# Kernel tuning notes

Hardware: AMD Instinct MI355X
Metric: run time of the kernel (lower is better)

The kernel has to match this reference:

```python
import jax, jax.numpy as jnp
import numpy as np

N = 65536        # total points across batch
NS = 16          # nsample (kNN neighbors)
D = 64           # d_model
FF = 64          # dim_feedforward width
CIN = 16         # input feature channels
EPS = 1e-5       # BatchNorm eps


def _bn_relu(x, g, b):
    # BatchNorm1d in training mode: per-channel stats over (N, L); x: (N, C, L)
    m = x.mean(axis=(0, 2), keepdims=True)
    v = x.var(axis=(0, 2), keepdims=True)
    return jax.nn.relu((x - m) * jax.lax.rsqrt(v + EPS) * g[None, :, None] + b[None, :, None])


def _dknn_layer(xyz, feats, knn_idx, knn_empty,
                wq, bq, wk, bk, w1, g1, b1, w2, g2, b2, wo, go, bo):
    # nhead = 1 -> single head uses the full d_model split
    Q = feats @ wq + bq                        # (N, D)
    K = feats @ wk + bk                        # (N, D)
    Kx = jnp.concatenate([K, xyz], axis=1)     # use_xyz=True -> (N, D+3)
    Qx = jnp.concatenate([Q, xyz], axis=1)     # (N, D+3)
    Kg = jnp.transpose(Kx[knn_idx], (0, 2, 1))  # irregular gather -> (N, D+3, NS)
    Qe = Qx[:, :, None]                        # (N, D+3, 1)
    x = jnp.concatenate([Kg - Qe, jnp.broadcast_to(Qe, Kg.shape)], axis=1)  # (N, 2*(D+3), NS)
    x = jnp.where(knn_empty[:, None, None], 0.0, x)   # empty-ball masking
    x = _bn_relu(jnp.einsum('ncs,cf->nfs', x, w1), g1, b1)  # Conv1d k=1 == channel matmul
    x = _bn_relu(jnp.einsum('ncs,cf->nfs', x, w2), g2, b2)
    x = jnp.max(x, axis=2, keepdims=True)      # max-pool over neighbors -> (N, FF, 1)
    x = _bn_relu(jnp.einsum('ncs,cf->nfs', x, wo), go, bo)  # out_conv
    return x[:, :, 0]                          # (N, D)


def setup_inputs() -> dict:
    key = jax.random.key(0)
    ks = jax.random.split(key, 16)
    inp = {
        'src_xyz': jax.random.normal(ks[0], (N, 3), jnp.float32) * 20.0,
        'src_feats': jax.random.normal(ks[1], (N, CIN), jnp.float32),
        'knn_idx': jax.random.randint(ks[2], (N, NS), 0, N, jnp.int32),
        'knn_empty': jax.random.randint(ks[3], (N,), 0, 20, jnp.int32) == 0,
    }
    k = 4
    cin = CIN
    for i in range(2):
        s = 1.0 / np.sqrt(cin)
        inp[f'l{i}_wq'] = jax.random.normal(ks[k], (cin, D), jnp.float32) * s; k += 1
        inp[f'l{i}_bq'] = jnp.zeros((D,), jnp.float32)
        inp[f'l{i}_wk'] = jax.random.normal(ks[k], (cin, D), jnp.float32) * s; k += 1
        inp[f'l{i}_bk'] = jnp.zeros((D,), jnp.float32)
        c = 2 * (D + 3)
        inp[f'l{i}_w1'] = jax.random.normal(ks[k], (c, FF), jnp.float32) * np.sqrt(2.0 / c); k += 1
        inp[f'l{i}_g1'] = jnp.ones((FF,), jnp.float32)
        inp[f'l{i}_b1'] = jnp.zeros((FF,), jnp.float32)
        inp[f'l{i}_w2'] = jax.random.normal(ks[k], (FF, FF), jnp.float32) * np.sqrt(2.0 / FF); k += 1
        inp[f'l{i}_g2'] = jnp.ones((FF,), jnp.float32)
        inp[f'l{i}_b2'] = jnp.zeros((FF,), jnp.float32)
        inp[f'l{i}_wo'] = jax.random.normal(ks[k], (FF, D), jnp.float32) * np.sqrt(2.0 / FF); k += 1
        inp[f'l{i}_go'] = jnp.ones((D,), jnp.float32)
        inp[f'l{i}_bo'] = jnp.zeros((D,), jnp.float32)
        cin = D
    return inp


def reference(src_xyz, src_feats, knn_idx, knn_empty,
              l0_wq, l0_bq, l0_wk, l0_bk, l0_w1, l0_g1, l0_b1, l0_w2, l0_g2, l0_b2, l0_wo, l0_go, l0_bo,
              l1_wq, l1_bq, l1_wk, l1_bk, l1_w1, l1_g1, l1_b1, l1_w2, l1_g2, l1_b2, l1_wo, l1_go, l1_bo):
    f = _dknn_layer(src_xyz, src_feats, knn_idx, knn_empty,
                    l0_wq, l0_bq, l0_wk, l0_bk, l0_w1, l0_g1, l0_b1, l0_w2, l0_g2, l0_b2, l0_wo, l0_go, l0_bo)
    f = _dknn_layer(src_xyz, f, knn_idx, knn_empty,
                    l1_wq, l1_bq, l1_wk, l1_bk, l1_w1, l1_g1, l1_b1, l1_w2, l1_g2, l1_b2, l1_wo, l1_go, l1_bo)
    return f
```

## Files before the change

kernel.cpp:

```cpp
#include <hip/hip_runtime.h>
#include <cstdint>

#define NPTS 65536
#define NS 16
#define EPSV 1e-5f

typedef __attribute__((ext_vector_type(8))) short bf16x8;
typedef __attribute__((ext_vector_type(4))) float f32x4;
typedef __attribute__((ext_vector_type(4))) unsigned int u32x4;
union FragU { u32x4 u; bf16x8 h; };

#define SUM1 0
#define SSQ1 64
#define SUM2 128
#define SSQ2 192
#define SUM3 256
#define SSQ3 320
#define WKA_OFF 832
#define WQBA_OFF (832+4096)
#define BKA_OFF  (832+8192)
#define BQBA_OFF (832+8192+64)
#define STATS_FLOATS (832+8192+128)

__device__ __forceinline__ void split2(float e0, float e1, unsigned int& hi, unsigned int& lo) {
    unsigned int u0 = __float_as_uint(e0), u1 = __float_as_uint(e1);
    unsigned int h0 = u0 & 0xFFFF0000u, h1 = u1 & 0xFFFF0000u;
    hi = (h0 >> 16) | h1;
    float l0f = e0 - __uint_as_float(h0);
    float l1f = e1 - __uint_as_float(h1);
    lo = (__float_as_uint(l0f) >> 16) | (__float_as_uint(l1f) & 0xFFFF0000u);
}

__global__ void k_mask(const uint32_t* emp32, uint8_t* mask) {
    int bad = 0;
    for (int w = threadIdx.x; w < 1024; w += 256) bad |= (emp32[w] > 1u) ? 1 : 0;
    __shared__ int sbad[4];
    unsigned long long b = __ballot(bad != 0);
    if ((threadIdx.x & 63) == 0) sbad[threadIdx.x >> 6] = (b != 0ull) ? 1 : 0;
    __syncthreads();
    int flag = sbad[0] | sbad[1] | sbad[2] | sbad[3];
    int i = blockIdx.x * 256 + threadIdx.x;
    uint8_t mv;
    if (flag) mv = (((const uint8_t*)emp32)[i] != 0);
    else      mv = (emp32[i] != 0u);
    mask[i] = mv;
}

__global__ void k0(const float* wq, const float* bq, const float* wk, const float* bk,
                   const float* w1, float* stats, int cin) {
    int f = threadIdx.x;
    int c = blockIdx.x;
    float a = 0.f, q = 0.f;
    for (int d = 0; d < 64; d++) {
        float A  = w1[d*64 + f];
        float Bm = w1[(67+d)*64 + f] - A;
        a = fmaf(wk[c*64 + d], A,  a);
        q = fmaf(wq[c*64 + d], Bm, q);
    }
    stats[WKA_OFF  + c*64 + f] = a;
    stats[WQBA_OFF + c*64 + f] = q;
    if (c == 0) {
        float ba = 0.f, bqv = 0.f;
        for (int d = 0; d < 64; d++) {
            float A  = w1[d*64 + f];
            float Bm = w1[(67+d)*64 + f] - A;
            ba  = fmaf(bk[d], A,  ba);
            bqv = fmaf(bq[d], Bm, bqv);
        }
        stats[BKA_OFF  + f] = ba;
        stats[BQBA_OFF + f] = bqv;
    }
}

__global__ void k1(const float* feats, const float* xyz, const float* w1,
                   const float* stats, float* KA, float* QBA, int cin) {
    int t = blockIdx.x * 256 + threadIdx.x;
    int f = t & 63, n = t >> 6;
    const float* Wka  = stats + WKA_OFF;
    const float* Wqba = stats + WQBA_OFF;
    float ka = stats[BKA_OFF + f], qb = stats[BQBA_OFF + f];
    for (int c = 0; c < cin; c++) {
        float fv = feats[n*cin + c];
        ka = fmaf(fv, Wka[c*64 + f],  ka);
        qb = fmaf(fv, Wqba[c*64 + f], qb);
    }
    #pragma unroll
    for (int x = 0; x < 3; x++) {
        float xv = xyz[n*3 + x];
        float a  = w1[(64+x)*64 + f];
        ka = fmaf(xv, a, ka);
        qb = fmaf(xv, w1[(131+x)*64 + f] - a, qb);
    }
    KA[n*64 + f]  = ka;
    QBA[n*64 + f] = qb;
}

__global__ void k2(const float* KA, const float* QBA, const int* knn,
                   const uint8_t* mask, float* stats) {
    int lane = threadIdx.x & 63;
    int wv   = threadIdx.x >> 6;
    float s0 = 0.f, s1 = 0.f;
    for (int n = blockIdx.x * 4 + wv; n < NPTS; n += gridDim.x * 4) {
        float msk = mask[n] ? 0.0f : 1.0f;
        int myidx = knn[n*16 + (lane & 15)];
        float q = QBA[n*64 + lane];
        #pragma unroll
        for (int s = 0; s < 16; s++) {
            int j = __shfl(myidx, s, 64);
            float y = msk * (KA[j*64 + lane] + q);
            s0 += y;
            s1 = fmaf(y, y, s1);
        }
    }
    __shared__ float red[8][64];
    red[wv][lane] = s0;
    red[4+wv][lane] = s1;
    __syncthreads();
    if (wv == 0) {
        atomicAdd(&stats[SUM1 + lane], red[0][lane]+red[1][lane]+red[2][lane]+red[3][lane]);
        atomicAdd(&stats[SSQ1 + lane], red[4][lane]+red[5][lane]+red[6][lane]+red[7][lane]);
    }
}

__global__ void __launch_bounds__(256) k4(const float* KA, const float* QBA, const int* knn,
                   const uint8_t* mask, const float* w2, const float* g1, const float* b1,
                   float* stats, float* y2max, float* y2min) {
    const int l    = threadIdx.x & 63;
    const int wv   = threadIdx.x >> 6;
    const int sidx = l & 15;
    const int g    = l >> 4;
    const int col  = sidx;

    float sc1v[16], sh1v[16];
    const float inv = 1.0f / ((float)NPTS * (float)NS);
    #pragma unroll
    for (int t = 0; t < 2; t++)
    #pragma unroll
    for (int i = 0; i < 8; i++) {
        int c = t*32 + g*8 + i;
        float m = stats[SUM1 + c] * inv;
        float v = fmaxf(stats[SSQ1 + c] * inv - m*m, 0.0f);
        float s = g1[c] * rsqrtf(v + EPSV);
        sc1v[t*8+i] = s;
        sh1v[t*8+i] = fmaf(-m, s, b1[c]);
    }

    unsigned int whu[2][4][4], wlu[2][4][4];
    #pragma unroll
    for (int t = 0; t < 2; t++)
    #pragma unroll
    for (int ft = 0; ft < 4; ft++)
    #pragma unroll
    for (int r = 0; r < 4; r++) {
        int k0i = t*32 + g*8 + 2*r;
        float e0 = w2[k0i*64 + ft*16 + col];
        float e1 = w2[(k0i+1)*64 + ft*16 + col];
        split2(e0, e1, whu[t][ft][r], wlu[t][ft][r]);
    }

    float s0t[4] = {0.f,0.f,0.f,0.f};
    float s1t[4] = {0.f,0.f,0.f,0.f};

    for (int n = blockIdx.x * 4 + wv; n < NPTS; n += gridDim.x * 4) {
        bool masked = mask[n] != 0;
        int j = knn[n*16 + sidx];

        f32x4 kaA = *(const f32x4*)(KA + j*64 + g*8);
        f32x4 kaB = *(const f32x4*)(KA + j*64 + g*8 + 4);
        f32x4 kaC = *(const f32x4*)(KA + j*64 + 32 + g*8);
        f32x4 kaD = *(const f32x4*)(KA + j*64 + 32 + g*8 + 4);
        f32x4 qA  = *(const f32x4*)(QBA + n*64 + g*8);
        f32x4 qB  = *(const f32x4*)(QBA + n*64 + g*8 + 4);
        f32x4 qC  = *(const f32x4*)(QBA + n*64 + 32 + g*8);
        f32x4 qD  = *(const f32x4*)(QBA + n*64 + 32 + g*8 + 4);

        float x[16];
        #pragma unroll
        for (int i = 0; i < 4; i++) {
            float y0 = masked ? 0.f : (kaA[i] + qA[i]);
            float y1 = masked ? 0.f : (kaB[i] + qB[i]);
            float y2 = masked ? 0.f : (kaC[i] + qC[i]);
            float y3 = masked ? 0.f : (kaD[i] + qD[i]);
            x[i]    = fmaxf(fmaf(sc1v[i],    y0, sh1v[i]),    0.0f);
            x[4+i]  = fmaxf(fmaf(sc1v[4+i],  y1, sh1v[4+i]),  0.0f);
            x[8+i]  = fmaxf(fmaf(sc1v[8+i],  y2, sh1v[8+i]),  0.0f);
            x[12+i] = fmaxf(fmaf(sc1v[12+i], y3, sh1v[12+i]), 0.0f);
        }

        unsigned int ahu[2][4], alu[2][4];
        #pragma unroll
        for (int t = 0; t < 2; t++)
        #pragma unroll
        for (int r = 0; r < 4; r++)
            split2(x[t*8 + 2*r], x[t*8 + 2*r + 1], ahu[t][r], alu[t][r]);

        f32x4 acc[4];
        #pragma unroll
        for (int ft = 0; ft < 4; ft++) acc[ft] = (f32x4){0.f,0.f,0.f,0.f};

        #pragma unroll
        for (int t = 0; t < 2; t++) {
            FragU ah, al;
            ah.u = (u32x4){ahu[t][0], ahu[t][1], ahu[t][2], ahu[t][3]};
            al.u = (u32x4){alu[t][0], alu[t][1], alu[t][2], alu[t][3]};
            #pragma unroll
            for (int ft = 0; ft < 4; ft++) {
                FragU bh, bl;
                bh.u = (u32x4){whu[t][ft][0], whu[t][ft][1], whu[t][ft][2], whu[t][ft][3]};
                bl.u = (u32x4){wlu[t][ft][0], wlu[t][ft][1], wlu[t][ft][2], wlu[t][ft][3]};
                acc[ft] = __builtin_amdgcn_mfma_f32_16x16x32_bf16(ah.h, bh.h, acc[ft], 0, 0, 0);
                acc[ft] = __builtin_amdgcn_mfma_f32_16x16x32_bf16(ah.h, bl.h, acc[ft], 0, 0, 0);
                acc[ft] = __builtin_amdgcn_mfma_f32_16x16x32_bf16(al.h, bh.h, acc[ft], 0, 0, 0);
            }
        }

        float tmax[4], tmin[4];
        #pragma unroll
        for (int ft = 0; ft < 4; ft++) {
            f32x4 d = acc[ft];
            float lmax = fmaxf(fmaxf(d[0], d[1]), fmaxf(d[2], d[3]));
            float lmin = fminf(fminf(d[0], d[1]), fminf(d[2], d[3]));
            s0t[ft] += (d[0] + d[1]) + (d[2] + d[3]);
            s1t[ft] += fmaf(d[0],d[0], fmaf(d[1],d[1], fmaf(d[2],d[2], d[3]*d[3])));
            lmax = fmaxf(lmax, __shfl_xor(lmax, 16, 64));
            lmax = fmaxf(lmax, __shfl_xor(lmax, 32, 64));
            lmin = fminf(lmin, __shfl_xor(lmin, 16, 64));
            lmin = fminf(lmin, __shfl_xor(lmin, 32, 64));
            tmax[ft] = lmax; tmin[ft] = lmin;
        }
        float mx = (g==0) ? tmax[0] : (g==1) ? tmax[1] : (g==2) ? tmax[2] : tmax[3];
        float mn = (g==0) ? tmin[0] : (g==1) ? tmin[1] : (g==2) ? tmin[2] : tmin[3];
        y2max[n*64 + l] = mx;
        y2min[n*64 + l] = mn;
    }

    #pragma unroll
    for (int ft = 0; ft < 4; ft++) {
        s0t[ft] += __shfl_xor(s0t[ft], 16, 64);
        s0t[ft] += __shfl_xor(s0t[ft], 32, 64);
        s1t[ft] += __shfl_xor(s1t[ft], 16, 64);
        s1t[ft] += __shfl_xor(s1t[ft], 32, 64);
    }
    float myS0 = (g==0) ? s0t[0] : (g==1) ? s0t[1] : (g==2) ? s0t[2] : s0t[3];
    float myS1 = (g==0) ? s1t[0] : (g==1) ? s1t[1] : (g==2) ? s1t[2] : s1t[3];
    __shared__ float red[8][64];
    red[wv][l] = myS0;
    red[4+wv][l] = myS1;
    __syncthreads();
    if (wv == 0) {
        atomicAdd(&stats[SUM2 + l], red[0][l]+red[1][l]+red[2][l]+red[3][l]);
        atomicAdd(&stats[SSQ2 + l], red[4][l]+red[5][l]+red[6][l]+red[7][l]);
    }
}

__global__ void k5(const float* y2max, const float* y2min, const float* wo,
                   const float* g2, const float* b2, float* stats, float* y3) {
    int lane = threadIdx.x & 63;
    int wv   = threadIdx.x >> 6;
    float woc[64];
    #pragma unroll
    for (int c = 0; c < 64; c++) woc[c] = wo[c*64 + lane];
    const float inv = 1.0f / ((float)NPTS * (float)NS);
    float m2 = stats[SUM2 + lane] * inv;
    float v2 = fmaxf(stats[SSQ2 + lane] * inv - m2*m2, 0.0f);
    float sc2 = g2[lane] * rsqrtf(v2 + EPSV);
    float sh2 = fmaf(-m2, sc2, b2[lane]);
    float s0 = 0.f, s1 = 0.f;
    for (int n = blockIdx.x * 4 + wv; n < NPTS; n += gridDim.x * 4) {
        float pre = (sc2 >= 0.0f) ? y2max[n*64 + lane] : y2min[n*64 + lane];
        float m = fmaxf(fmaf(sc2, pre, sh2), 0.0f);
        float acc = 0.f;
        #pragma unroll
        for (int c = 0; c < 64; c++) {
            float xc = __uint_as_float(__builtin_amdgcn_readlane(__float_as_uint(m), c));
            acc = fmaf(xc, woc[c], acc);
        }
        y3[n*64 + lane] = acc;
        s0 += acc;
        s1 = fmaf(acc, acc, s1);
    }
    __shared__ float red[8][64];
    red[wv][lane] = s0;
    red[4+wv][lane] = s1;
    __syncthreads();
    if (wv == 0) {
        atomicAdd(&stats[SUM3 + lane], red[0][lane]+red[1][lane]+red[2][lane]+red[3][lane]);
        atomicAdd(&stats[SSQ3 + lane], red[4][lane]+red[5][lane]+red[6][lane]+red[7][lane]);
    }
}

__global__ void k6(const float* y3, const float* stats, const float* go, const float* bo,
                   float* out) {
    int i = blockIdx.x * 256 + threadIdx.x;
    int f = i & 63;
    const float inv = 1.0f / (float)NPTS;
    float m = stats[SUM3 + f] * inv;
    float v = fmaxf(stats[SSQ3 + f] * inv - m*m, 0.0f);
    float s = go[f] * rsqrtf(v + EPSV);
    float sh = fmaf(-m, s, bo[f]);
    out[i] = fmaxf(fmaf(s, y3[i], sh), 0.0f);
}

extern "C" void kernel_launch(void* const* d_in, const int* in_sizes, int n_in,
                              void* d_out, int out_size, void* d_ws, size_t ws_size,
                              hipStream_t stream) {
    const float* xyz    = (const float*)d_in[0];
    const float* feats0 = (const float*)d_in[1];
    const int*   knn    = (const int*)d_in[2];
    const void*  empty  = d_in[3];
    float* ws = (float*)d_ws;
    const size_t N64 = (size_t)NPTS * 64;
    float* KA    = ws;
    float* QBA   = ws + N64;
    float* Y2MAX = ws + 2*N64;
    float* Y2MIN = ws + 3*N64;
    float* stats = ws + 4*N64;
    uint8_t* mask = (uint8_t*)(stats + STATS_FLOATS);
    float* out = (float*)d_out;

    k_mask<<<NPTS/256, 256, 0, stream>>>((const uint32_t*)empty, mask);

    const float* feats = feats0;
    int cin = 16;
    for (int L = 0; L < 2; L++) {
        const float* const* p = (const float* const*)(d_in + 4 + L*13);
        const float* wq = p[0];  const float* bq = p[1];
        const float* wk = p[2];  const float* bk = p[3];
        const float* w1 = p[4];  const float* g1 = p[5];  const float* b1 = p[6];
        const float* w2 = p[7];  const float* g2 = p[8];  const float* b2 = p[9];
        const float* wo = p[10]; const float* go = p[11]; const float* bo = p[12];

        hipMemsetAsync(stats, 0, 384 * sizeof(float), stream);
        k0<<<cin, 64, 0, stream>>>(wq, bq, wk, bk, w1, stats, cin);
        k1<<<NPTS*64/256, 256, 0, stream>>>(feats, xyz, w1, stats, KA, QBA, cin);
        k2<<<1024, 256, 0, stream>>>(KA, QBA, knn, mask, stats);
        k4<<<1024, 256, 0, stream>>>(KA, QBA, knn, mask, w2, g1, b1, stats, Y2MAX, Y2MIN);
        k5<<<1024, 256, 0, stream>>>(Y2MAX, Y2MIN, wo, g2, b2, stats, KA);
        k6<<<NPTS*64/256, 256, 0, stream>>>(KA, stats, go, bo, out);

        feats = out;
        cin = 64;
    }
}
```

Before: 653.0 us.

## Use MFMA for projection and output conv, fuse layer-0 final BN into next layer

The per-point projection (k1) and the output conv (k5) now run as split-bf16 MFMA tile matmuls instead of scalar FMA loops. The layer-0 final BatchNorm+ReLU is folded into the layer-1 projection input, which removes one elementwise kernel. The k2 stats reduction now skips masked points, uses vectorized loads and shuffle reductions, and grid sizes change to 2048. Together these aim to cut ALU time and launch count, at the cost of more register pressure and bf16 split precision error.

```diff
diff --git a/kernel.cpp b/kernel.cpp
--- a/kernel.cpp
+++ b/kernel.cpp
@@ -16,11 +16,11 @@
 #define SSQ2 192
 #define SUM3 256
 #define SSQ3 320
-#define WKA_OFF 832
-#define WQBA_OFF (832+4096)
-#define BKA_OFF  (832+8192)
-#define BQBA_OFF (832+8192+64)
-#define STATS_FLOATS (832+8192+128)
+#define WKAOF 0
+#define WQBAOF 4096
+#define BKAOF 8192
+#define BQBAOF 8256
+#define WFOLD_FLOATS 8320
 
 __device__ __forceinline__ void split2(float e0, float e1, unsigned int& hi, unsigned int& lo) {
     unsigned int u0 = __float_as_uint(e0), u1 = __float_as_uint(e1);
@@ -47,7 +47,7 @@
 }
 
 __global__ void k0(const float* wq, const float* bq, const float* wk, const float* bk,
-                   const float* w1, float* stats, int cin) {
+                   const float* w1, float* wfold, int cin) {
     int f = threadIdx.x;
     int c = blockIdx.x;
     float a = 0.f, q = 0.f;
@@ -57,8 +57,8 @@
         a = fmaf(wk[c*64 + d], A,  a);
         q = fmaf(wq[c*64 + d], Bm, q);
     }
-    stats[WKA_OFF  + c*64 + f] = a;
-    stats[WQBA_OFF + c*64 + f] = q;
+    wfold[WKAOF  + c*64 + f] = a;
+    wfold[WQBAOF + c*64 + f] = q;
     if (c == 0) {
         float ba = 0.f, bqv = 0.f;
         for (int d = 0; d < 64; d++) {
@@ -67,58 +67,206 @@
             ba  = fmaf(bk[d], A,  ba);
             bqv = fmaf(bq[d], Bm, bqv);
         }
-        stats[BKA_OFF  + f] = ba;
-        stats[BQBA_OFF + f] = bqv;
-    }
-}
-
-__global__ void k1(const float* feats, const float* xyz, const float* w1,
-                   const float* stats, float* KA, float* QBA, int cin) {
-    int t = blockIdx.x * 256 + threadIdx.x;
-    int f = t & 63, n = t >> 6;
-    const float* Wka  = stats + WKA_OFF;
-    const float* Wqba = stats + WQBA_OFF;
-    float ka = stats[BKA_OFF + f], qb = stats[BQBA_OFF + f];
-    for (int c = 0; c < cin; c++) {
-        float fv = feats[n*cin + c];
-        ka = fmaf(fv, Wka[c*64 + f],  ka);
-        qb = fmaf(fv, Wqba[c*64 + f], qb);
-    }
-    #pragma unroll
-    for (int x = 0; x < 3; x++) {
-        float xv = xyz[n*3 + x];
-        float a  = w1[(64+x)*64 + f];
-        ka = fmaf(xv, a, ka);
-        qb = fmaf(xv, w1[(131+x)*64 + f] - a, qb);
-    }
-    KA[n*64 + f]  = ka;
-    QBA[n*64 + f] = qb;
-}
-
-__global__ void k2(const float* KA, const float* QBA, const int* knn,
-                   const uint8_t* mask, float* stats) {
-    int lane = threadIdx.x & 63;
-    int wv   = threadIdx.x >> 6;
-    float s0 = 0.f, s1 = 0.f;
+        wfold[BKAOF  + f] = ba;
+        wfold[BQBAOF + f] = bqv;
+    }
+}
+
+template<int CIN, bool PREBN>
+__global__ void __launch_bounds__(256) k1m(const float* __restrict__ feats, const float* __restrict__ xyz,
+                    const float* __restrict__ w1, const float* __restrict__ wfold,
+                    const float* __restrict__ statsPrev, const float* __restrict__ goP,
+                    const float* __restrict__ boP,
+                    float* __restrict__ KA, float* __restrict__ QBA) {
+    const int l = threadIdx.x & 63;
+    const int wv = threadIdx.x >> 6;
+    const int sidx = l & 15;
+    const int g = l >> 4;
+    const int col = sidx;
+    constexpr int NT = (CIN == 64) ? 2 : 1;
+
+    unsigned int bh[NT][2][4], bl[NT][2][4];
+    #pragma unroll
+    for (int t = 0; t < NT; t++)
+    #pragma unroll
+    for (int fl = 0; fl < 2; fl++) {
+        int f128 = (wv*2 + fl)*16 + col;
+        const float* W = (f128 < 64) ? (wfold + WKAOF) : (wfold + WQBAOF);
+        int f = (f128 < 64) ? f128 : f128 - 64;
+        #pragma unroll
+        for (int r = 0; r < 4; r++) {
+            int c0 = t*32 + g*8 + 2*r;
+            float e0 = 0.f, e1 = 0.f;
+            if (CIN == 64 || g < 2) {
+                e0 = W[c0*64 + f];
+                e1 = W[(c0+1)*64 + f];
+            }
+            split2(e0, e1, bh[t][fl][r], bl[t][fl][r]);
+        }
+    }
+    unsigned int xbh[2][4], xbl[2][4];
+    float biasf[2];
+    #pragma unroll
+    for (int fl = 0; fl < 2; fl++) {
+        int f128 = (wv*2 + fl)*16 + col;
+        float A0, A1, A2;
+        if (f128 < 64) {
+            A0 = w1[64*64 + f128]; A1 = w1[65*64 + f128]; A2 = w1[66*64 + f128];
+            biasf[fl] = wfold[BKAOF + f128];
+        } else {
+            int f = f128 - 64;
+            A0 = w1[131*64 + f] - w1[64*64 + f];
+            A1 = w1[132*64 + f] - w1[65*64 + f];
+            A2 = w1[133*64 + f] - w1[66*64 + f];
+            biasf[fl] = wfold[BQBAOF + f];
+        }
+        split2(A0, A1, xbh[fl][0], xbl[fl][0]);
+        split2(A2, 0.f, xbh[fl][1], xbl[fl][1]);
+        xbh[fl][2] = 0; xbh[fl][3] = 0; xbl[fl][2] = 0; xbl[fl][3] = 0;
+    }
+    float scP[NT*8], shP[NT*8];
+    if (PREBN) {
+        const float invN = 1.0f / (float)NPTS;
+        #pragma unroll
+        for (int t = 0; t < NT; t++)
+        #pragma unroll
+        for (int i = 0; i < 8; i++) {
+            int c = t*32 + g*8 + i;
+            float m = statsPrev[SUM3 + c] * invN;
+            float v = fmaxf(statsPrev[SSQ3 + c] * invN - m*m, 0.0f);
+            float s = goP[c] * rsqrtf(v + EPSV);
+            scP[t*8+i] = s;
+            shP[t*8+i] = fmaf(-m, s, boP[c]);
+        }
+    }
+
+    for (int tile = blockIdx.x; tile < NPTS/16; tile += gridDim.x) {
+        int p = tile*16 + sidx;
+        unsigned int ahu[NT][4], alu[NT][4];
+        #pragma unroll
+        for (int t = 0; t < NT; t++) {
+            float xv[8];
+            if (CIN == 64) {
+                f32x4 a0 = *(const f32x4*)(feats + (size_t)p*64 + t*32 + g*8);
+                f32x4 a1 = *(const f32x4*)(feats + (size_t)p*64 + t*32 + g*8 + 4);
+                #pragma unroll
+                for (int i = 0; i < 4; i++) { xv[i] = a0[i]; xv[4+i] = a1[i]; }
+                if (PREBN) {
+                    #pragma unroll
+                    for (int i = 0; i < 8; i++)
+                        xv[i] = fmaxf(fmaf(scP[t*8+i], xv[i], shP[t*8+i]), 0.0f);
+                }
+            } else {
+                if (g < 2) {
+                    f32x4 a0 = *(const f32x4*)(feats + (size_t)p*16 + g*8);
+                    f32x4 a1 = *(const f32x4*)(feats + (size_t)p*16 + g*8 + 4);
+                    #pragma unroll
+                    for (int i = 0; i < 4; i++) { xv[i] = a0[i]; xv[4+i] = a1[i]; }
+                } else {
+                    #pragma unroll
+                    for (int i = 0; i < 8; i++) xv[i] = 0.f;
+                }
+            }
+            #pragma unroll
+            for (int r = 0; r < 4; r++) split2(xv[2*r], xv[2*r+1], ahu[t][r], alu[t][r]);
+        }
+        unsigned int xah[4] = {0,0,0,0}, xal[4] = {0,0,0,0};
+        if (g == 0) {
+            float x0 = xyz[p*3], x1 = xyz[p*3+1], x2 = xyz[p*3+2];
+            split2(x0, x1, xah[0], xal[0]);
+            split2(x2, 0.f, xah[1], xal[1]);
+        }
+        f32x4 acc[2];
+        #pragma unroll
+        for (int fl = 0; fl < 2; fl++)
+            acc[fl] = (f32x4){biasf[fl], biasf[fl], biasf[fl], biasf[fl]};
+        #pragma unroll
+        for (int t = 0; t < NT; t++) {
+            FragU ah, al;
+            ah.u = (u32x4){ahu[t][0], ahu[t][1], ahu[t][2], ahu[t][3]};
+            al.u = (u32x4){alu[t][0], alu[t][1], alu[t][2], alu[t][3]};
+            #pragma unroll
+            for (int fl = 0; fl < 2; fl++) {
+                FragU Bh, Bl;
+                Bh.u = (u32x4){bh[t][fl][0], bh[t][fl][1], bh[t][fl][2], bh[t][fl][3]};
+                Bl.u = (u32x4){bl[t][fl][0], bl[t][fl][1], bl[t][fl][2], bl[t][fl][3]};
+                acc[fl] = __builtin_amdgcn_mfma_f32_16x16x32_bf16(ah.h, Bh.h, acc[fl], 0, 0, 0);
+                acc[fl] = __builtin_amdgcn_mfma_f32_16x16x32_bf16(ah.h, Bl.h, acc[fl], 0, 0, 0);
+                acc[fl] = __builtin_amdgcn_mfma_f32_16x16x32_bf16(al.h, Bh.h, acc[fl], 0, 0, 0);
+            }
+        }
+        {
+            FragU ah, al;
+            ah.u = (u32x4){xah[0], xah[1], xah[2], xah[3]};
+            al.u = (u32x4){xal[0], xal[1], xal[2], xal[3]};
+            #pragma unroll
+            for (int fl = 0; fl < 2; fl++) {
+                FragU Bh, Bl;
+                Bh.u = (u32x4){xbh[fl][0], xbh[fl][1], xbh[fl][2], xbh[fl][3]};
+                Bl.u = (u32x4){xbl[fl][0], xbl[fl][1], xbl[fl][2], xbl[fl][3]};
+                acc[fl] = __builtin_amdgcn_mfma_f32_16x16x32_bf16(ah.h, Bh.h, acc[fl], 0, 0, 0);
+                acc[fl] = __builtin_amdgcn_mfma_f32_16x16x32_bf16(ah.h, Bl.h, acc[fl], 0, 0, 0);
+                acc[fl] = __builtin_amdgcn_mfma_f32_16x16x32_bf16(al.h, Bh.h, acc[fl], 0, 0, 0);
+            }
+        }
+        #pragma unroll
+        for (int fl = 0; fl < 2; fl++) {
+            int f128 = (wv*2 + fl)*16 + col;
+            #pragma unroll
+            for (int r = 0; r < 4; r++) {
+                int po = tile*16 + g*4 + r;
+                float v = acc[fl][r];
+                if (f128 < 64) KA[(size_t)po*64 + f128] = v;
+                else           QBA[(size_t)po*64 + (f128-64)] = v;
+            }
+        }
+    }
+}
+
+__global__ void __launch_bounds__(256) k2(const float* __restrict__ KA, const float* __restrict__ QBA,
+                   const int* __restrict__ knn, const uint8_t* __restrict__ mask, float* stats) {
+    const int l = threadIdx.x & 63;
+    const int wv = threadIdx.x >> 6;
+    const int s = l & 15;
+    const int g = l >> 4;
+    float s0[16], s1[16];
+    #pragma unroll
+    for (int i = 0; i < 16; i++) { s0[i] = 0.f; s1[i] = 0.f; }
     for (int n = blockIdx.x * 4 + wv; n < NPTS; n += gridDim.x * 4) {
-        float msk = mask[n] ? 0.0f : 1.0f;
-        int myidx = knn[n*16 + (lane & 15)];
-        float q = QBA[n*64 + lane];
-        #pragma unroll
-        for (int s = 0; s < 16; s++) {
-            int j = __shfl(myidx, s, 64);
-            float y = msk * (KA[j*64 + lane] + q);
-            s0 += y;
-            s1 = fmaf(y, y, s1);
-        }
-    }
-    __shared__ float red[8][64];
-    red[wv][lane] = s0;
-    red[4+wv][lane] = s1;
+        if (mask[n]) continue;
+        int j = knn[n*16 + s];
+        const float* kap = KA + (size_t)j*64 + g*16;
+        const float* qbp = QBA + (size_t)n*64 + g*16;
+        #pragma unroll
+        for (int q = 0; q < 4; q++) {
+            f32x4 ka = *(const f32x4*)(kap + q*4);
+            f32x4 qb = *(const f32x4*)(qbp + q*4);
+            #pragma unroll
+            for (int e = 0; e < 4; e++) {
+                float y = ka[e] + qb[e];
+                s0[q*4+e] += y;
+                s1[q*4+e] = fmaf(y, y, s1[q*4+e]);
+            }
+        }
+    }
+    #pragma unroll
+    for (int i = 0; i < 16; i++) {
+        #pragma unroll
+        for (int d = 1; d < 16; d <<= 1) {
+            s0[i] += __shfl_xor(s0[i], d, 64);
+            s1[i] += __shfl_xor(s1[i], d, 64);
+        }
+    }
+    __shared__ float r0[4][64], r1[4][64];
+    if (s == 0) {
+        #pragma unroll
+        for (int i = 0; i < 16; i++) { r0[wv][g*16+i] = s0[i]; r1[wv][g*16+i] = s1[i]; }
+    }
     __syncthreads();
-    if (wv == 0) {
-        atomicAdd(&stats[SUM1 + lane], red[0][lane]+red[1][lane]+red[2][lane]+red[3][lane]);
-        atomicAdd(&stats[SSQ1 + lane], red[4][lane]+red[5][lane]+red[6][lane]+red[7][lane]);
+    int tid = threadIdx.x;
+    if (tid < 64) {
+        atomicAdd(&stats[SUM1 + tid], r0[0][tid]+r0[1][tid]+r0[2][tid]+r0[3][tid]);
+        atomicAdd(&stats[SSQ1 + tid], r1[0][tid]+r1[1][tid]+r1[2][tid]+r1[3][tid]);
     }
 }
 
@@ -165,14 +313,14 @@
         bool masked = mask[n] != 0;
         int j = knn[n*16 + sidx];
 
-        f32x4 kaA = *(const f32x4*)(KA + j*64 + g*8);
-        f32x4 kaB = *(const f32x4*)(KA + j*64 + g*8 + 4);
-        f32x4 kaC = *(const f32x4*)(KA + j*64 + 32 + g*8);
-        f32x4 kaD = *(const f32x4*)(KA + j*64 + 32 + g*8 + 4);
-        f32x4 qA  = *(const f32x4*)(QBA + n*64 + g*8);
-        f32x4 qB  = *(const f32x4*)(QBA + n*64 + g*8 + 4);
-        f32x4 qC  = *(const f32x4*)(QBA + n*64 + 32 + g*8);
-        f32x4 qD  = *(const f32x4*)(QBA + n*64 + 32 + g*8 + 4);
+        f32x4 kaA = *(const f32x4*)(KA + (size_t)j*64 + g*8);
+        f32x4 kaB = *(const f32x4*)(KA + (size_t)j*64 + g*8 + 4);
+        f32x4 kaC = *(const f32x4*)(KA + (size_t)j*64 + 32 + g*8);
+        f32x4 kaD = *(const f32x4*)(KA + (size_t)j*64 + 32 + g*8 + 4);
+        f32x4 qA  = *(const f32x4*)(QBA + (size_t)n*64 + g*8);
+        f32x4 qB  = *(const f32x4*)(QBA + (size_t)n*64 + g*8 + 4);
+        f32x4 qC  = *(const f32x4*)(QBA + (size_t)n*64 + 32 + g*8);
+        f32x4 qD  = *(const f32x4*)(QBA + (size_t)n*64 + 32 + g*8 + 4);
 
         float x[16];
         #pragma unroll
@@ -205,12 +353,12 @@
             al.u = (u32x4){alu[t][0], alu[t][1], alu[t][2], alu[t][3]};
             #pragma unroll
             for (int ft = 0; ft < 4; ft++) {
-                FragU bh, bl;
-                bh.u = (u32x4){whu[t][ft][0], whu[t][ft][1], whu[t][ft][2], whu[t][ft][3]};
-                bl.u = (u32x4){wlu[t][ft][0], wlu[t][ft][1], wlu[t][ft][2], wlu[t][ft][3]};
-                acc[ft] = __builtin_amdgcn_mfma_f32_16x16x32_bf16(ah.h, bh.h, acc[ft], 0, 0, 0);
-                acc[ft] = __builtin_amdgcn_mfma_f32_16x16x32_bf16(ah.h, bl.h, acc[ft], 0, 0, 0);
-                acc[ft] = __builtin_amdgcn_mfma_f32_16x16x32_bf16(al.h, bh.h, acc[ft], 0, 0, 0);
+                FragU bhf, blf;
+                bhf.u = (u32x4){whu[t][ft][0], whu[t][ft][1], whu[t][ft][2], whu[t][ft][3]};
+                blf.u = (u32x4){wlu[t][ft][0], wlu[t][ft][1], wlu[t][ft][2], wlu[t][ft][3]};
+                acc[ft] = __builtin_amdgcn_mfma_f32_16x16x32_bf16(ah.h, bhf.h, acc[ft], 0, 0, 0);
+                acc[ft] = __builtin_amdgcn_mfma_f32_16x16x32_bf16(ah.h, blf.h, acc[ft], 0, 0, 0);
+                acc[ft] = __builtin_amdgcn_mfma_f32_16x16x32_bf16(al.h, bhf.h, acc[ft], 0, 0, 0);
             }
         }
 
@@ -230,8 +378,8 @@
         }
         float mx = (g==0) ? tmax[0] : (g==1) ? tmax[1] : (g==2) ? tmax[2] : tmax[3];
         float mn = (g==0) ? tmin[0] : (g==1) ? tmin[1] : (g==2) ? tmin[2] : tmin[3];
-        y2max[n*64 + l] = mx;
-        y2min[n*64 + l] = mn;
+        y2max[(size_t)n*64 + l] = mx;
+        y2min[(size_t)n*64 + l] = mn;
     }
 
     #pragma unroll
@@ -253,44 +401,93 @@
     }
 }
 
-__global__ void k5(const float* y2max, const float* y2min, const float* wo,
-                   const float* g2, const float* b2, float* stats, float* y3) {
-    int lane = threadIdx.x & 63;
-    int wv   = threadIdx.x >> 6;
-    float woc[64];
-    #pragma unroll
-    for (int c = 0; c < 64; c++) woc[c] = wo[c*64 + lane];
+__global__ void __launch_bounds__(256) k5m(const float* __restrict__ y2max, const float* __restrict__ y2min,
+                    const float* __restrict__ wo, const float* __restrict__ g2, const float* __restrict__ b2,
+                    float* stats, float* __restrict__ y3) {
+    const int l = threadIdx.x & 63;
+    const int wv = threadIdx.x >> 6;
+    const int sidx = l & 15;
+    const int g = l >> 4;
+    const int ft = wv;
+
+    unsigned int bh[2][4], bl[2][4];
+    #pragma unroll
+    for (int t = 0; t < 2; t++)
+    #pragma unroll
+    for (int r = 0; r < 4; r++) {
+        int c0 = t*32 + g*8 + 2*r;
+        split2(wo[c0*64 + ft*16 + sidx], wo[(c0+1)*64 + ft*16 + sidx], bh[t][r], bl[t][r]);
+    }
+    float sc2v[16], sh2v[16];
     const float inv = 1.0f / ((float)NPTS * (float)NS);
-    float m2 = stats[SUM2 + lane] * inv;
-    float v2 = fmaxf(stats[SSQ2 + lane] * inv - m2*m2, 0.0f);
-    float sc2 = g2[lane] * rsqrtf(v2 + EPSV);
-    float sh2 = fmaf(-m2, sc2, b2[lane]);
-    float s0 = 0.f, s1 = 0.f;
-    for (int n = blockIdx.x * 4 + wv; n < NPTS; n += gridDim.x * 4) {
-        float pre = (sc2 >= 0.0f) ? y2max[n*64 + lane] : y2min[n*64 + lane];
-        float m = fmaxf(fmaf(sc2, pre, sh2), 0.0f);
-        float acc = 0.f;
-        #pragma unroll
-        for (int c = 0; c < 64; c++) {
-            float xc = __uint_as_float(__builtin_amdgcn_readlane(__float_as_uint(m), c));
-            acc = fmaf(xc, woc[c], acc);
-        }
-        y3[n*64 + lane] = acc;
-        s0 += acc;
-        s1 = fmaf(acc, acc, s1);
-    }
-    __shared__ float red[8][64];
-    red[wv][lane] = s0;
-    red[4+wv][lane] = s1;
+    #pragma unroll
+    for (int t = 0; t < 2; t++)
+    #pragma unroll
+    for (int i = 0; i < 8; i++) {
+        int c = t*32 + g*8 + i;
+        float m = stats[SUM2 + c] * inv;
+        float v = fmaxf(stats[SSQ2 + c] * inv - m*m, 0.0f);
+        float s = g2[c] * rsqrtf(v + EPSV);
+        sc2v[t*8+i] = s;
+        sh2v[t*8+i] = fmaf(-m, s, b2[c]);
+    }
+    float s0a = 0.f, s1a = 0.f;
+    for (int tile = blockIdx.x; tile < NPTS/16; tile += gridDim.x) {
+        int p = tile*16 + sidx;
+        unsigned int ahu[2][4], alu[2][4];
+        #pragma unroll
+        for (int t = 0; t < 2; t++) {
+            f32x4 mx0 = *(const f32x4*)(y2max + (size_t)p*64 + t*32 + g*8);
+            f32x4 mx1 = *(const f32x4*)(y2max + (size_t)p*64 + t*32 + g*8 + 4);
+            f32x4 mn0 = *(const f32x4*)(y2min + (size_t)p*64 + t*32 + g*8);
+            f32x4 mn1 = *(const f32x4*)(y2min + (size_t)p*64 + t*32 + g*8 + 4);
+            float mval[8];
+            #pragma unroll
+            for (int i = 0; i < 4; i++) {
+                float sc = sc2v[t*8+i];
+                float pre = (sc >= 0.f) ? mx0[i] : mn0[i];
+                mval[i] = fmaxf(fmaf(sc, pre, sh2v[t*8+i]), 0.0f);
+                float sc2 = sc2v[t*8+4+i];
+                float pre2 = (sc2 >= 0.f) ? mx1[i] : mn1[i];
+                mval[4+i] = fmaxf(fmaf(sc2, pre2, sh2v[t*8+4+i]), 0.0f);
+            }
+            #pragma unroll
+            for (int r = 0; r < 4; r++) split2(mval[2*r], mval[2*r+1], ahu[t][r], alu[t][r]);
+        }
+        f32x4 acc = (f32x4){0.f,0.f,0.f,0.f};
+        #pragma unroll
+        for (int t = 0; t < 2; t++) {
+            FragU ah, al, Bh, Bl;
+            ah.u = (u32x4){ahu[t][0], ahu[t][1], ahu[t][2], ahu[t][3]};
+            al.u = (u32x4){alu[t][0], alu[t][1], alu[t][2], alu[t][3]};
+            Bh.u = (u32x4){bh[t][0], bh[t][1], bh[t][2], bh[t][3]};
+            Bl.u = (u32x4){bl[t][0], bl[t][1], bl[t][2], bl[t][3]};
+            acc = __builtin_amdgcn_mfma_f32_16x16x32_bf16(ah.h, Bh.h, acc, 0, 0, 0);
+            acc = __builtin_amdgcn_mfma_f32_16x16x32_bf16(ah.h, Bl.h, acc, 0, 0, 0);
+            acc = __builtin_amdgcn_mfma_f32_16x16x32_bf16(al.h, Bh.h, acc, 0, 0, 0);
+        }
+        #pragma unroll
+        for (int r = 0; r < 4; r++) {
+            int po = tile*16 + g*4 + r;
+            float v = acc[r];
+            y3[(size_t)po*64 + ft*16 + sidx] = v;
+            s0a += v;
+            s1a = fmaf(v, v, s1a);
+        }
+    }
+    s0a += __shfl_xor(s0a, 16, 64); s0a += __shfl_xor(s0a, 32, 64);
+    s1a += __shfl_xor(s1a, 16, 64); s1a += __shfl_xor(s1a, 32, 64);
+    __shared__ float r0[64], r1[64];
+    if (l < 16) { r0[wv*16 + sidx] = s0a; r1[wv*16 + sidx] = s1a; }
     __syncthreads();
-    if (wv == 0) {
-        atomicAdd(&stats[SUM3 + lane], red[0][lane]+red[1][lane]+red[2][lane]+red[3][lane]);
-        atomicAdd(&stats[SSQ3 + lane], red[4][lane]+red[5][lane]+red[6][lane]+red[7][lane]);
-    }
-}
-
-__global__ void k6(const float* y3, const float* stats, const float* go, const float* bo,
-                   float* out) {
+    int tid = threadIdx.x;
+    if (tid < 64) {
+        atomicAdd(&stats[SUM3 + tid], r0[tid]);
+        atomicAdd(&stats[SSQ3 + tid], r1[tid]);
+    }
+}
+
+__global__ void k6(float* y3, const float* stats, const float* go, const float* bo) {
     int i = blockIdx.x * 256 + threadIdx.x;
     int f = i & 63;
     const float inv = 1.0f / (float)NPTS;
@@ -298,7 +495,7 @@
     float v = fmaxf(stats[SSQ3 + f] * inv - m*m, 0.0f);
     float s = go[f] * rsqrtf(v + EPSV);
     float sh = fmaf(-m, s, bo[f]);
-    out[i] = fmaxf(fmaf(s, y3[i], sh), 0.0f);
+    y3[i] = fmaxf(fmaf(s, y3[i], sh), 0.0f);
 }
 
 extern "C" void kernel_launch(void* const* d_in, const int* in_sizes, int n_in,
@@ -315,30 +512,35 @@
     float* Y2MAX = ws + 2*N64;
     float* Y2MIN = ws + 3*N64;
     float* stats = ws + 4*N64;
-    uint8_t* mask = (uint8_t*)(stats + STATS_FLOATS);
+    float* wfold = stats + 1024;
+    uint8_t* mask = (uint8_t*)(wfold + WFOLD_FLOATS);
     float* out = (float*)d_out;
 
+    hipMemsetAsync(stats, 0, 1024 * sizeof(float), stream);
     k_mask<<<NPTS/256, 256, 0, stream>>>((const uint32_t*)empty, mask);
 
-    const float* feats = feats0;
-    int cin = 16;
-    for (int L = 0; L < 2; L++) {
-        const float* const* p = (const float* const*)(d_in + 4 + L*13);
-        const float* wq = p[0];  const float* bq = p[1];
-        const float* wk = p[2];  const float* bk = p[3];
-        const float* w1 = p[4];  const float* g1 = p[5];  const float* b1 = p[6];
-        const float* w2 = p[7];  const float* g2 = p[8];  const float* b2 = p[9];
-        const float* wo = p[10]; const float* go = p[11]; const float* bo = p[12];
-
-        hipMemsetAsync(stats, 0, 384 * sizeof(float), stream);
-        k0<<<cin, 64, 0, stream>>>(wq, bq, wk, bk, w1, stats, cin);
-        k1<<<NPTS*64/256, 256, 0, stream>>>(feats, xyz, w1, stats, KA, QBA, cin);
-        k2<<<1024, 256, 0, stream>>>(KA, QBA, knn, mask, stats);
-        k4<<<1024, 256, 0, stream>>>(KA, QBA, knn, mask, w2, g1, b1, stats, Y2MAX, Y2MIN);
-        k5<<<1024, 256, 0, stream>>>(Y2MAX, Y2MIN, wo, g2, b2, stats, KA);
-        k6<<<NPTS*64/256, 256, 0, stream>>>(KA, stats, go, bo, out);
-
-        feats = out;
-        cin = 64;
-    }
-}
+    const float* const* p0 = (const float* const*)(d_in + 4);
+    const float* const* p1 = (const float* const*)(d_in + 4 + 13);
+
+    {
+        const float* const* p = p0;
+        float* sl = stats;
+        k0<<<16, 64, 0, stream>>>(p[0], p[1], p[2], p[3], p[4], wfold, 16);
+        k1m<16, false><<<1024, 256, 0, stream>>>(feats0, xyz, p[4], wfold,
+                                                 sl, p[11], p[12], KA, QBA);
+        k2<<<2048, 256, 0, stream>>>(KA, QBA, knn, mask, sl);
+        k4<<<2048, 256, 0, stream>>>(KA, QBA, knn, mask, p[7], p[5], p[6], sl, Y2MAX, Y2MIN);
+        k5m<<<2048, 256, 0, stream>>>(Y2MAX, Y2MIN, p[10], p[8], p[9], sl, out);
+    }
+    {
+        const float* const* p = p1;
+        float* sl = stats + 512;
+        k0<<<64, 64, 0, stream>>>(p[0], p[1], p[2], p[3], p[4], wfold, 64);
+        k1m<64, true><<<1024, 256, 0, stream>>>(out, xyz, p[4], wfold,
+                                                stats, p0[11], p0[12], KA, QBA);
+        k2<<<2048, 256, 0, stream>>>(KA, QBA, knn, mask, sl);
+        k4<<<2048, 256, 0, stream>>>(KA, QBA, knn, mask, p[7], p[5], p[6], sl, Y2MAX, Y2MIN);
+        k5m<<<2048, 256, 0, stream>>>(Y2MAX, Y2MIN, p[10], p[8], p[9], sl, out);
+        k6<<<NPTS*64/256, 256, 0, stream>>>(out, sl, p[11], p[12]);
+    }
+}
```

Result: faster. 621.3 us (-4.9%).
